# Optimization experiments

Hardware: AMD Instinct MI355X
Metric: run time of the kernel (lower is better)

The kernel has to match this reference:

```python
import jax, jax.numpy as jnp
import numpy as np

B, T, HID = 4, 2048, 2048
H, DK, DV = 16, 128, 128
EPS = 1e-5


def setup_inputs() -> dict:
    key = jax.random.key(0)
    ks = jax.random.split(key, 14)
    w = lambda k, shape, s=0.02: jax.random.normal(k, shape, jnp.float32) * s
    return dict(
        hidden_states=jax.random.normal(ks[0], (B, T, HID), jnp.float32),
        recurrent_state=jnp.zeros((B, H, DK, DV), jnp.float32),
        q_w=w(ks[1], (H * DK, HID)),
        k_w=w(ks[2], (H * DK, HID)),
        v_w=w(ks[3], (H * DV, HID)),
        f_w0=w(ks[4], (DV, HID)),
        f_w1=w(ks[5], (H * DK, DV)),
        b_w=w(ks[6], (H, HID)),
        A_log=jnp.log(jax.random.uniform(ks[7], (H,), jnp.float32, 1.0, 16.0)),
        dt_bias=w(ks[8], (H * DK,), 0.1),
        g_w0=w(ks[9], (DV, HID)),
        g_w1=w(ks[10], (H * DV, DV)),
        g_b1=w(ks[11], (H * DV,), 0.1),
        o_norm_weight=jnp.ones((DV,), jnp.float32),
        o_w=w(ks[12], (HID, H * DV)),
    )


def _l2norm(x):
    return x * jax.lax.rsqrt(jnp.sum(x * x, -1, keepdims=True) + 1e-6)


def _kda_scan(q, k, v, g, beta, S0):
    # time-major inputs: q,k,g [T,B,H,DK]; v [T,B,H,DV]; beta [T,B,H]; S0 [B,H,DK,DV]
    scale = DK ** -0.5

    def step(S, inp):
        qt, kt, vt, gt, bt = inp
        S = S * jnp.exp(gt)[..., None]                      # per-key-dim decay
        kv = jnp.einsum('bhk,bhkv->bhv', kt, S)             # current readout for k
        delta = (vt - kv) * bt[..., None]                   # beta-weighted correction
        S = S + kt[..., :, None] * delta[..., None, :]      # rank-1 delta update
        ot = jnp.einsum('bhk,bhkv->bhv', qt * scale, S)
        return S, ot

    S, o = jax.lax.scan(step, S0, (q, k, v, g, beta))
    return o, S


def reference(hidden_states, recurrent_state, q_w, k_w, v_w, f_w0, f_w1, b_w,
              A_log, dt_bias, g_w0, g_w1, g_b1, o_norm_weight, o_w):
    h = hidden_states
    q = jax.nn.silu(h @ q_w.T).reshape(B, T, H, DK)
    k = jax.nn.silu(h @ k_w.T).reshape(B, T, H, DK)
    v = jax.nn.silu(h @ v_w.T).reshape(B, T, H, DV)
    # fused_kda_gate: g = -exp(A_log) * softplus(g + dt_bias), per key channel
    g = ((h @ f_w0.T) @ f_w1.T).reshape(B, T, H, DK)
    g = -jnp.exp(A_log)[None, None, :, None] * jax.nn.softplus(g + dt_bias.reshape(H, DK))
    beta = jax.nn.sigmoid(h @ b_w.T)  # [B,T,H]
    q = _l2norm(q)
    k = _l2norm(k)
    tm = lambda x: jnp.swapaxes(x, 0, 1)  # -> time-major
    o, S = _kda_scan(tm(q), tm(k), tm(v), tm(g), tm(beta), recurrent_state)
    o = jnp.swapaxes(o, 0, 1)  # [B,T,H,DV]
    factor = ((h @ g_w0.T) @ g_w1.T + g_b1).reshape(B, T, H, DV)
    # FusedRMSNormGated(activation='sigmoid'): rmsnorm then sigmoid gate
    o = o * jax.lax.rsqrt(jnp.mean(o * o, -1, keepdims=True) + EPS)
    o = o * o_norm_weight * jax.nn.sigmoid(factor)
    out = o.reshape(B, T, H * DV) @ o_w.T
    return out, S
```

## Files before the change

kernel.cpp:

```cpp
#include <hip/hip_runtime.h>
#include <math.h>


typedef short short8 __attribute__((ext_vector_type(8)));
typedef float f32x4 __attribute__((ext_vector_type(4)));
typedef unsigned short ushort_t;

enum { ACT_NONE = 0, ACT_SILU = 1, ACT_SIGMOID = 2, ACT_KDAGATE_EXP = 3 };

__device__ __forceinline__ unsigned short f32_to_bf16(float f) {
  unsigned int u = __float_as_uint(f);
  u += 0x7FFFu + ((u >> 16) & 1u);
  return (unsigned short)(u >> 16);
}

__device__ __forceinline__ float epi_act(float x, int act, int n,
                                         const float* bias, const float* A_log,
                                         const float* dt_bias) {
  if (bias) x += bias[n];
  if (act == ACT_SILU) {
    x = x / (1.f + __expf(-x));
  } else if (act == ACT_SIGMOID) {
    x = 1.f / (1.f + __expf(-x));
  } else if (act == ACT_KDAGATE_EXP) {
    float y = x + dt_bias[n];
    float sp = fmaxf(y, 0.f) + log1pf(__expf(-fabsf(y)));
    x = __expf(-__expf(A_log[n >> 7]) * sp);
  }
  return x;
}

__device__ __forceinline__ void gld_lds16(const void* g, void* l) {
  __builtin_amdgcn_global_load_lds(
      (const __attribute__((address_space(1))) unsigned int*)g,
      (__attribute__((address_space(3))) unsigned int*)l, 16, 0, 0);
}

__device__ __forceinline__ float row16_sum(float x) {
  x += __int_as_float(__builtin_amdgcn_update_dpp(0, __float_as_int(x), 0xB1, 0xF, 0xF, true));
  x += __int_as_float(__builtin_amdgcn_update_dpp(0, __float_as_int(x), 0x4E, 0xF, 0xF, true));
  x += __int_as_float(__builtin_amdgcn_update_dpp(0, __float_as_int(x), 0x141, 0xF, 0xF, true));
  x += __int_as_float(__builtin_amdgcn_update_dpp(0, __float_as_int(x), 0x140, 0xF, 0xF, true));
  return x;
}

__device__ __forceinline__ void unpk8(const uint4 p, float* f) {
  f[0] = __uint_as_float(p.x << 16); f[1] = __uint_as_float(p.x & 0xFFFF0000u);
  f[2] = __uint_as_float(p.y << 16); f[3] = __uint_as_float(p.y & 0xFFFF0000u);
  f[4] = __uint_as_float(p.z << 16); f[5] = __uint_as_float(p.z & 0xFFFF0000u);
  f[6] = __uint_as_float(p.w << 16); f[7] = __uint_as_float(p.w & 0xFFFF0000u);
}

__global__ __launch_bounds__(256) void gemm_bf16_nt(
    const ushort_t* __restrict__ A, const ushort_t* __restrict__ W,
    float* __restrict__ Cf, ushort_t* __restrict__ Cb,
    int M, int N, int K, int act, const float* __restrict__ bias,
    const float* __restrict__ A_log, const float* __restrict__ dt_bias) {
  __shared__ alignas(16) ushort_t As[4096];
  __shared__ alignas(16) ushort_t Bs[4096];
  const int tid = threadIdx.x;
  const int wv = tid >> 6, ln = tid & 63;
  const int bm = blockIdx.y * 128, bn = blockIdx.x * 128;
  const int wm = wv >> 1, wn = wv & 1;

  const int srow = tid >> 2;
  const int skg = (tid & 3) ^ ((srow >> 1) & 3);
  const size_t ag0 = (size_t)(bm + srow) * K + skg * 8;
  const size_t ag1 = ag0 + (size_t)64 * K;
  const size_t bg0 = (size_t)(bn + srow) * K + skg * 8;
  const size_t bg1 = bg0 + (size_t)64 * K;
  char* const lA = (char*)As;
  char* const lB = (char*)Bs;
  const int wbase = wv * 1024;

  const int fr = ln & 15, fq = ln >> 4;
  const int pg = fq ^ ((fr >> 1) & 3);
  int aoff[4], boff[4];
#pragma unroll
  for (int i = 0; i < 4; i++) {
    aoff[i] = (wm * 64 + i * 16 + fr) * 64 + pg * 16;
    boff[i] = (wn * 64 + i * 16 + fr) * 64 + pg * 16;
  }

  f32x4 acc[4][4];
#pragma unroll
  for (int i = 0; i < 4; i++)
#pragma unroll
    for (int j = 0; j < 4; j++) {
      acc[i][j][0] = 0.f; acc[i][j][1] = 0.f; acc[i][j][2] = 0.f; acc[i][j][3] = 0.f;
    }

  for (int k0 = 0; k0 < K; k0 += 32) {
    gld_lds16(A + ag0 + k0, lA + wbase);
    gld_lds16(A + ag1 + k0, lA + 4096 + wbase);
    gld_lds16(W + bg0 + k0, lB + wbase);
    gld_lds16(W + bg1 + k0, lB + 4096 + wbase);
    __syncthreads();
    short8 af[4], bf[4];
#pragma unroll
    for (int i = 0; i < 4; i++) af[i] = *(const short8*)(lA + aoff[i]);
#pragma unroll
    for (int i = 0; i < 4; i++) bf[i] = *(const short8*)(lB + boff[i]);
#pragma unroll
    for (int i = 0; i < 4; i++)
#pragma unroll
      for (int j = 0; j < 4; j++)
        acc[i][j] = __builtin_amdgcn_mfma_f32_16x16x32_bf16(af[i], bf[j], acc[i][j], 0, 0, 0);
    __syncthreads();
  }

  const int cc = ln & 15, cq = ln >> 4;
#pragma unroll
  for (int i = 0; i < 4; i++) {
#pragma unroll
    for (int r = 0; r < 4; r++) {
      const int gm = bm + wm * 64 + i * 16 + cq * 4 + r;
#pragma unroll
      for (int j = 0; j < 4; j++) {
        const int gn = bn + wn * 64 + j * 16 + cc;
        float x = epi_act(acc[i][j][r], act, gn, bias, A_log, dt_bias);
        if (Cb) Cb[(size_t)gm * N + gn] = f32_to_bf16(x);
        else    Cf[(size_t)gm * N + gn] = x;
      }
    }
  }
}

#define BM 128
#define BN 128
#define BKK 8
__global__ __launch_bounds__(256) void gemm_nt(
    const float* __restrict__ A, const float* __restrict__ W,
    float* __restrict__ C, int M, int N, int K, int act) {
  __shared__ alignas(16) float Asf[BKK][BM + 4];
  __shared__ alignas(16) float Wsf[BKK][BN + 4];
  const int tid = threadIdx.x;
  const int bm = blockIdx.y * BM;
  const int bn = blockIdx.x * BN;
  const int tn = tid & 15, tm = tid >> 4;
  const int lrow = tid >> 1;
  const int lk = (tid & 1) * 4;

  float acc[8][8];
#pragma unroll
  for (int i = 0; i < 8; i++)
#pragma unroll
    for (int j = 0; j < 8; j++) acc[i][j] = 0.f;

  for (int k0 = 0; k0 < K; k0 += BKK) {
    const float4 a4 = *(const float4*)&A[(size_t)(bm + lrow) * K + k0 + lk];
    float4 w4 = make_float4(0.f, 0.f, 0.f, 0.f);
    if (bn + lrow < N) w4 = *(const float4*)&W[(size_t)(bn + lrow) * K + k0 + lk];
    __syncthreads();
    Asf[lk + 0][lrow] = a4.x; Asf[lk + 1][lrow] = a4.y;
    Asf[lk + 2][lrow] = a4.z; Asf[lk + 3][lrow] = a4.w;
    Wsf[lk + 0][lrow] = w4.x; Wsf[lk + 1][lrow] = w4.y;
    Wsf[lk + 2][lrow] = w4.z; Wsf[lk + 3][lrow] = w4.w;
    __syncthreads();
#pragma unroll
    for (int kk = 0; kk < BKK; kk++) {
      const float4 a0 = *(const float4*)&Asf[kk][tm * 8];
      const float4 a1 = *(const float4*)&Asf[kk][tm * 8 + 4];
      const float4 b0 = *(const float4*)&Wsf[kk][tn * 8];
      const float4 b1 = *(const float4*)&Wsf[kk][tn * 8 + 4];
      const float av[8] = {a0.x, a0.y, a0.z, a0.w, a1.x, a1.y, a1.z, a1.w};
      const float bv[8] = {b0.x, b0.y, b0.z, b0.w, b1.x, b1.y, b1.z, b1.w};
#pragma unroll
      for (int i = 0; i < 8; i++)
#pragma unroll
        for (int j = 0; j < 8; j++) acc[i][j] = fmaf(av[i], bv[j], acc[i][j]);
    }
  }
#pragma unroll
  for (int i = 0; i < 8; i++) {
    const int m = bm + tm * 8 + i;
#pragma unroll
    for (int j = 0; j < 8; j++) {
      const int n = bn + tn * 8 + j;
      if (n < N) {
        float x = acc[i][j];
        if (act == ACT_SIGMOID) x = 1.f / (1.f + __expf(-x));
        C[(size_t)m * N + n] = x;
      }
    }
  }
}

__global__ __launch_bounds__(256) void cast_bf16(const float* __restrict__ x,
                                                 ushort_t* __restrict__ y, int n) {
  const int i = (blockIdx.x * 256 + threadIdx.x) * 4;
  if (i >= n) return;
  const float4 v = *(const float4*)&x[i];
  union { ushort_t u[4]; uint2 v2; } o;
  o.u[0] = f32_to_bf16(v.x); o.u[1] = f32_to_bf16(v.y);
  o.u[2] = f32_to_bf16(v.z); o.u[3] = f32_to_bf16(v.w);
  *(uint2*)&y[i] = o.v2;
}

__global__ __launch_bounds__(64) void l2norm_bf16(const float* __restrict__ x,
                                                  ushort_t* __restrict__ y, float scale) {
  const size_t base = (size_t)blockIdx.x * 128;
  const int lane = threadIdx.x;
  const float a = x[base + lane];
  const float b = x[base + lane + 64];
  float ss = fmaf(a, a, b * b);
#pragma unroll
  for (int m = 1; m < 64; m <<= 1) ss += __shfl_xor(ss, m);
  const float r = rsqrtf(ss + 1e-6f) * scale;
  y[base + lane] = f32_to_bf16(a * r);
  y[base + lane + 64] = f32_to_bf16(b * r);
}

struct StepRegs { uint4 kp, qp; float4 g0, g1; float vv, bb; };

__global__ __launch_bounds__(64) void kda_scan(
    const ushort_t* __restrict__ q, const ushort_t* __restrict__ k,
    const float* __restrict__ v, const float* __restrict__ ge,
    const float* __restrict__ beta, const float* __restrict__ S0,
    float* __restrict__ o, float* __restrict__ S_out) {
  const int bid = blockIdx.x;
  const int bh = (((bid >> 3) & 7) << 3) | (bid & 7);
  const int cg = bid >> 6;
  const int h = bh & 15, b = bh >> 4;
  const int ln = threadIdx.x;
  const int cl = ln >> 4, kg = ln & 15;
  const int col = cg * 4 + cl;
  const int kof = kg * 8;

  const size_t s_base = (size_t)bh * (128 * 128);
  float S[8];
#pragma unroll
  for (int j = 0; j < 8; j++) S[j] = S0[s_base + (size_t)(kof + j) * 128 + col];

  const size_t rb = (size_t)b * (2048 * 2048) + (size_t)h * 128;
  const size_t bbase = (size_t)(b * 2048) * 16 + h;

  StepRegs sr[4];
#pragma unroll
  for (int s = 0; s < 4; s++) {
    const size_t a = rb + (size_t)s * 2048;
    sr[s].kp = *(const uint4*)&k[a + kof];
    sr[s].qp = *(const uint4*)&q[a + kof];
    sr[s].g0 = *(const float4*)&ge[a + kof];
    sr[s].g1 = *(const float4*)&ge[a + kof + 4];
    sr[s].vv = v[a + col];
    sr[s].bb = beta[bbase + (size_t)s * 16];
  }

  for (int t = 0; t < 2048; t += 4) {
#pragma unroll
    for (int s = 0; s < 4; s++) {
      const int tt = t + s;
      float kf[8], qf[8];
      unpk8(sr[s].kp, kf);
      unpk8(sr[s].qp, qf);
      const float4 g0 = sr[s].g0, g1 = sr[s].g1;
      float p0 = 0.f, p1 = 0.f;
      S[0] *= g0.x; p0 = fmaf(kf[0], S[0], p0);
      S[1] *= g0.y; p1 = fmaf(kf[1], S[1], p1);
      S[2] *= g0.z; p0 = fmaf(kf[2], S[2], p0);
      S[3] *= g0.w; p1 = fmaf(kf[3], S[3], p1);
      S[4] *= g1.x; p0 = fmaf(kf[4], S[4], p0);
      S[5] *= g1.y; p1 = fmaf(kf[5], S[5], p1);
      S[6] *= g1.z; p0 = fmaf(kf[6], S[6], p0);
      S[7] *= g1.w; p1 = fmaf(kf[7], S[7], p1);
      const float p = row16_sum(p0 + p1);
      const float delta = (sr[s].vv - p) * sr[s].bb;
      float o0 = 0.f, o1 = 0.f;
      S[0] = fmaf(kf[0], delta, S[0]); o0 = fmaf(qf[0], S[0], o0);
      S[1] = fmaf(kf[1], delta, S[1]); o1 = fmaf(qf[1], S[1], o1);
      S[2] = fmaf(kf[2], delta, S[2]); o0 = fmaf(qf[2], S[2], o0);
      S[3] = fmaf(kf[3], delta, S[3]); o1 = fmaf(qf[3], S[3], o1);
      S[4] = fmaf(kf[4], delta, S[4]); o0 = fmaf(qf[4], S[4], o0);
      S[5] = fmaf(kf[5], delta, S[5]); o1 = fmaf(qf[5], S[5], o1);
      S[6] = fmaf(kf[6], delta, S[6]); o0 = fmaf(qf[6], S[6], o0);
      S[7] = fmaf(kf[7], delta, S[7]); o1 = fmaf(qf[7], S[7], o1);
      const float op = row16_sum(o0 + o1);
      if (kg == 0) o[rb + (size_t)tt * 2048 + col] = op;
      const int tn = (tt + 4 < 2048) ? tt + 4 : 2047;
      const size_t a = rb + (size_t)tn * 2048;
      sr[s].kp = *(const uint4*)&k[a + kof];
      sr[s].qp = *(const uint4*)&q[a + kof];
      sr[s].g0 = *(const float4*)&ge[a + kof];
      sr[s].g1 = *(const float4*)&ge[a + kof + 4];
      sr[s].vv = v[a + col];
      sr[s].bb = beta[bbase + (size_t)tn * 16];
    }
  }
#pragma unroll
  for (int j = 0; j < 8; j++)
    S_out[s_base + (size_t)(kof + j) * 128 + col] = S[j];
}

__global__ __launch_bounds__(128) void gate_rmsnorm(
    const float* __restrict__ o, const float* __restrict__ factor,
    const float* __restrict__ w, ushort_t* __restrict__ out) {
  const size_t base = (size_t)blockIdx.x * 128;
  const int vi = threadIdx.x;
  const float x = o[base + vi];
  float ss = x * x;
#pragma unroll
  for (int m = 1; m < 64; m <<= 1) ss += __shfl_xor(ss, m);
  __shared__ float red[2];
  if ((vi & 63) == 0) red[vi >> 6] = ss;
  __syncthreads();
  const float tot = red[0] + red[1];
  const float r = rsqrtf(tot * (1.f / 128.f) + 1e-5f);
  const float f = factor[base + vi];
  const float sig = 1.f / (1.f + __expf(-f));
  out[base + vi] = f32_to_bf16(x * r * w[vi] * sig);
}

extern "C" void kernel_launch(void* const* d_in, const int* in_sizes, int n_in,
                              void* d_out, int out_size, void* d_ws, size_t ws_size,
                              hipStream_t stream) {
  const float* h    = (const float*)d_in[0];
  const float* S0   = (const float*)d_in[1];
  const float* q_w  = (const float*)d_in[2];
  const float* k_w  = (const float*)d_in[3];
  const float* v_w  = (const float*)d_in[4];
  const float* f_w0 = (const float*)d_in[5];
  const float* f_w1 = (const float*)d_in[6];
  const float* b_w  = (const float*)d_in[7];
  const float* A_log  = (const float*)d_in[8];
  const float* dt_b   = (const float*)d_in[9];
  const float* g_w0 = (const float*)d_in[10];
  const float* g_w1 = (const float*)d_in[11];
  const float* g_b1 = (const float*)d_in[12];
  const float* o_nw = (const float*)d_in[13];
  const float* o_w  = (const float*)d_in[14];

  float* outp = (float*)d_out;
  float* Sout = outp + (size_t)8192 * 2048;

  const size_t BIG = (size_t)8192 * 2048;
  float* ws = (float*)d_ws;
  float* vbuf = ws;
  float* obuf = vbuf + BIG;
  float* betab = obuf + BIG;
  ushort_t* qb16 = (ushort_t*)(betab + (size_t)8192 * 16);
  ushort_t* kb16 = qb16 + BIG;
  ushort_t* hb   = kb16 + BIG;
  ushort_t* wq   = hb + BIG;
  ushort_t* wk   = wq + (size_t)2048 * 2048;
  ushort_t* wv   = wk + (size_t)2048 * 2048;
  ushort_t* wo   = wv + (size_t)2048 * 2048;
  ushort_t* wf0  = wo + (size_t)2048 * 2048;
  ushort_t* wg0  = wf0 + (size_t)128 * 2048;
  ushort_t* wf1  = wg0 + (size_t)128 * 2048;
  ushort_t* wg1  = wf1 + (size_t)2048 * 128;
  ushort_t* fpreb = wg1 + (size_t)2048 * 128;
  ushort_t* gpreb = fpreb + (size_t)8192 * 128;

  const dim3 blk(256);
  const dim3 gbig(16, 64);
  const dim3 gnarrow(1, 64);

  cast_bf16<<<16384, blk, 0, stream>>>(h, hb, 8192 * 2048);
  cast_bf16<<<4096, blk, 0, stream>>>(q_w, wq, 2048 * 2048);
  cast_bf16<<<4096, blk, 0, stream>>>(k_w, wk, 2048 * 2048);
  cast_bf16<<<4096, blk, 0, stream>>>(v_w, wv, 2048 * 2048);
  cast_bf16<<<4096, blk, 0, stream>>>(o_w, wo, 2048 * 2048);
  cast_bf16<<<256, blk, 0, stream>>>(f_w0, wf0, 128 * 2048);
  cast_bf16<<<256, blk, 0, stream>>>(g_w0, wg0, 128 * 2048);
  cast_bf16<<<256, blk, 0, stream>>>(f_w1, wf1, 2048 * 128);
  cast_bf16<<<256, blk, 0, stream>>>(g_w1, wg1, 2048 * 128);

  gemm_bf16_nt<<<gbig, blk, 0, stream>>>(hb, wq, obuf, nullptr, 8192, 2048, 2048, ACT_SILU, nullptr, nullptr, nullptr);
  l2norm_bf16<<<131072, 64, 0, stream>>>(obuf, qb16, 0.08838834764831845f);
  gemm_bf16_nt<<<gbig, blk, 0, stream>>>(hb, wk, obuf, nullptr, 8192, 2048, 2048, ACT_SILU, nullptr, nullptr, nullptr);
  l2norm_bf16<<<131072, 64, 0, stream>>>(obuf, kb16, 1.0f);
  gemm_bf16_nt<<<gbig, blk, 0, stream>>>(hb, wv, vbuf, nullptr, 8192, 2048, 2048, ACT_SILU, nullptr, nullptr, nullptr);
  gemm_bf16_nt<<<gnarrow, blk, 0, stream>>>(hb, wf0, nullptr, fpreb, 8192, 128, 2048, ACT_NONE, nullptr, nullptr, nullptr);
  gemm_bf16_nt<<<gnarrow, blk, 0, stream>>>(hb, wg0, nullptr, gpreb, 8192, 128, 2048, ACT_NONE, nullptr, nullptr, nullptr);
  gemm_nt<<<gnarrow, blk, 0, stream>>>(h, b_w, betab, 8192, 16, 2048, ACT_SIGMOID);
  gemm_bf16_nt<<<gbig, blk, 0, stream>>>(fpreb, wf1, outp, nullptr, 8192, 2048, 128, ACT_KDAGATE_EXP, nullptr, A_log, dt_b);
  kda_scan<<<2048, 64, 0, stream>>>(qb16, kb16, vbuf, outp, betab, S0, obuf, Sout);
  gemm_bf16_nt<<<gbig, blk, 0, stream>>>(gpreb, wg1, outp, nullptr, 8192, 2048, 128, ACT_NONE, g_b1, nullptr, nullptr);
  gate_rmsnorm<<<131072, 128, 0, stream>>>(obuf, outp, o_nw, qb16);
  gemm_bf16_nt<<<gbig, blk, 0, stream>>>(qb16, wo, outp, nullptr, 8192, 2048, 2048, ACT_NONE, nullptr, nullptr, nullptr);
}
```

Measured before the change: 2.130 ms.

## Fuse QKV projections with L2 norm epilogue, merge low-rank GEMMs, restructure scan

Merges the three Q/K/V projection GEMMs into one launch over concatenated weights. The SiLU and per-row L2 normalization are now done in the GEMM epilogue through an LDS cross-wave reduction, which removes the separate l2norm kernels. The f/g low-rank down-projections and the beta projection are combined into one bf16 GEMM, replacing the fp32 SIMT GEMM for beta. The scan now reads q and k as fp32 and computes the output as q·S_decayed + (q·k)·delta, so the three reductions can proceed together. The gated RMSNorm is rewritten to process several rows per block with vectorized accesses. In exchange, q and k buffers move from bf16 to fp32, which doubles their traffic in the scan.

```diff
diff --git a/kernel.cpp b/kernel.cpp
--- a/kernel.cpp
+++ b/kernel.cpp
@@ -6,7 +6,7 @@
 typedef float f32x4 __attribute__((ext_vector_type(4)));
 typedef unsigned short ushort_t;
 
-enum { ACT_NONE = 0, ACT_SILU = 1, ACT_SIGMOID = 2, ACT_KDAGATE_EXP = 3 };
+enum { M_PLAIN = 0, M_QKV = 1, M_LOWRANK = 2, M_GATE = 3, M_FACTOR = 4 };
 
 __device__ __forceinline__ unsigned short f32_to_bf16(float f) {
   unsigned int u = __float_as_uint(f);
@@ -14,21 +14,7 @@
   return (unsigned short)(u >> 16);
 }
 
-__device__ __forceinline__ float epi_act(float x, int act, int n,
-                                         const float* bias, const float* A_log,
-                                         const float* dt_bias) {
-  if (bias) x += bias[n];
-  if (act == ACT_SILU) {
-    x = x / (1.f + __expf(-x));
-  } else if (act == ACT_SIGMOID) {
-    x = 1.f / (1.f + __expf(-x));
-  } else if (act == ACT_KDAGATE_EXP) {
-    float y = x + dt_bias[n];
-    float sp = fmaxf(y, 0.f) + log1pf(__expf(-fabsf(y)));
-    x = __expf(-__expf(A_log[n >> 7]) * sp);
-  }
-  return x;
-}
+__device__ __forceinline__ float silu(float x) { return x / (1.f + __expf(-x)); }
 
 __device__ __forceinline__ void gld_lds16(const void* g, void* l) {
   __builtin_amdgcn_global_load_lds(
@@ -44,20 +30,16 @@
   return x;
 }
 
-__device__ __forceinline__ void unpk8(const uint4 p, float* f) {
-  f[0] = __uint_as_float(p.x << 16); f[1] = __uint_as_float(p.x & 0xFFFF0000u);
-  f[2] = __uint_as_float(p.y << 16); f[3] = __uint_as_float(p.y & 0xFFFF0000u);
-  f[4] = __uint_as_float(p.z << 16); f[5] = __uint_as_float(p.z & 0xFFFF0000u);
-  f[6] = __uint_as_float(p.w << 16); f[7] = __uint_as_float(p.w & 0xFFFF0000u);
-}
-
-__global__ __launch_bounds__(256) void gemm_bf16_nt(
+__global__ __launch_bounds__(256) void gemm_bf16(
     const ushort_t* __restrict__ A, const ushort_t* __restrict__ W,
-    float* __restrict__ Cf, ushort_t* __restrict__ Cb,
-    int M, int N, int K, int act, const float* __restrict__ bias,
-    const float* __restrict__ A_log, const float* __restrict__ dt_bias) {
+    int M, int N, int K, int mode,
+    float* __restrict__ f0, float* __restrict__ f1, float* __restrict__ f2,
+    ushort_t* __restrict__ b0, ushort_t* __restrict__ b1,
+    const float* __restrict__ bias, const float* __restrict__ A_log,
+    const float* __restrict__ dt_bias) {
   __shared__ alignas(16) ushort_t As[4096];
   __shared__ alignas(16) ushort_t Bs[4096];
+  __shared__ float l2s[2][128];
   const int tid = threadIdx.x;
   const int wv = tid >> 6, ln = tid & 63;
   const int bm = blockIdx.y * 128, bn = blockIdx.x * 128;
@@ -110,80 +92,94 @@
   }
 
   const int cc = ln & 15, cq = ln >> 4;
-#pragma unroll
-  for (int i = 0; i < 4; i++) {
+
+  if (mode == M_QKV) {
+#pragma unroll
+    for (int i = 0; i < 4; i++)
+#pragma unroll
+      for (int j = 0; j < 4; j++)
+#pragma unroll
+        for (int r = 0; r < 4; r++) acc[i][j][r] = silu(acc[i][j][r]);
+    const bool isqk = (bn < 4096);
+    float invr[4][4];
+    if (isqk) {
+      const float scale = (bn < 2048) ? 0.08838834764831845f : 1.0f;
+#pragma unroll
+      for (int i = 0; i < 4; i++)
+#pragma unroll
+        for (int r = 0; r < 4; r++) {
+          float ss = 0.f;
+#pragma unroll
+          for (int j = 0; j < 4; j++) ss = fmaf(acc[i][j][r], acc[i][j][r], ss);
+          ss = row16_sum(ss);
+          if (cc == 0) l2s[wn][wm * 64 + i * 16 + cq * 4 + r] = ss;
+        }
+      __syncthreads();
+#pragma unroll
+      for (int i = 0; i < 4; i++)
+#pragma unroll
+        for (int r = 0; r < 4; r++) {
+          const int rl = wm * 64 + i * 16 + cq * 4 + r;
+          invr[i][r] = rsqrtf(l2s[0][rl] + l2s[1][rl] + 1e-6f) * scale;
+        }
+    } else {
+#pragma unroll
+      for (int i = 0; i < 4; i++)
+#pragma unroll
+        for (int r = 0; r < 4; r++) invr[i][r] = 1.f;
+    }
+    float* dst = (bn < 2048) ? f0 : ((bn < 4096) ? f1 : f2);
+    const int nb = bn & 2047;
+#pragma unroll
+    for (int i = 0; i < 4; i++)
+#pragma unroll
+      for (int r = 0; r < 4; r++) {
+        const int gm = bm + wm * 64 + i * 16 + cq * 4 + r;
+#pragma unroll
+        for (int j = 0; j < 4; j++) {
+          const int gn = nb + wn * 64 + j * 16 + cc;
+          dst[(size_t)gm * 2048 + gn] = acc[i][j][r] * invr[i][r];
+        }
+      }
+    return;
+  }
+
+  if (mode == M_LOWRANK) {
+#pragma unroll
+    for (int i = 0; i < 4; i++)
+#pragma unroll
+      for (int r = 0; r < 4; r++) {
+        const int gm = bm + wm * 64 + i * 16 + cq * 4 + r;
+#pragma unroll
+        for (int j = 0; j < 4; j++) {
+          const int gn = bn + wn * 64 + j * 16 + cc;
+          const float x = acc[i][j][r];
+          if (gn < 128) b0[(size_t)gm * 128 + gn] = f32_to_bf16(x);
+          else if (gn < 256) b1[(size_t)gm * 128 + (gn - 128)] = f32_to_bf16(x);
+          else if (gn < 272) f0[(size_t)gm * 16 + (gn - 256)] = 1.f / (1.f + __expf(-x));
+        }
+      }
+    return;
+  }
+
+#pragma unroll
+  for (int i = 0; i < 4; i++)
 #pragma unroll
     for (int r = 0; r < 4; r++) {
       const int gm = bm + wm * 64 + i * 16 + cq * 4 + r;
 #pragma unroll
       for (int j = 0; j < 4; j++) {
         const int gn = bn + wn * 64 + j * 16 + cc;
-        float x = epi_act(acc[i][j][r], act, gn, bias, A_log, dt_bias);
-        if (Cb) Cb[(size_t)gm * N + gn] = f32_to_bf16(x);
-        else    Cf[(size_t)gm * N + gn] = x;
+        float x = acc[i][j][r];
+        if (mode == M_FACTOR) x += bias[gn];
+        else if (mode == M_GATE) {
+          const float y = x + dt_bias[gn];
+          const float sp = fmaxf(y, 0.f) + log1pf(__expf(-fabsf(y)));
+          x = __expf(-__expf(A_log[gn >> 7]) * sp);
+        }
+        f0[(size_t)gm * N + gn] = x;
       }
     }
-  }
-}
-
-#define BM 128
-#define BN 128
-#define BKK 8
-__global__ __launch_bounds__(256) void gemm_nt(
-    const float* __restrict__ A, const float* __restrict__ W,
-    float* __restrict__ C, int M, int N, int K, int act) {
-  __shared__ alignas(16) float Asf[BKK][BM + 4];
-  __shared__ alignas(16) float Wsf[BKK][BN + 4];
-  const int tid = threadIdx.x;
-  const int bm = blockIdx.y * BM;
-  const int bn = blockIdx.x * BN;
-  const int tn = tid & 15, tm = tid >> 4;
-  const int lrow = tid >> 1;
-  const int lk = (tid & 1) * 4;
-
-  float acc[8][8];
-#pragma unroll
-  for (int i = 0; i < 8; i++)
-#pragma unroll
-    for (int j = 0; j < 8; j++) acc[i][j] = 0.f;
-
-  for (int k0 = 0; k0 < K; k0 += BKK) {
-    const float4 a4 = *(const float4*)&A[(size_t)(bm + lrow) * K + k0 + lk];
-    float4 w4 = make_float4(0.f, 0.f, 0.f, 0.f);
-    if (bn + lrow < N) w4 = *(const float4*)&W[(size_t)(bn + lrow) * K + k0 + lk];
-    __syncthreads();
-    Asf[lk + 0][lrow] = a4.x; Asf[lk + 1][lrow] = a4.y;
-    Asf[lk + 2][lrow] = a4.z; Asf[lk + 3][lrow] = a4.w;
-    Wsf[lk + 0][lrow] = w4.x; Wsf[lk + 1][lrow] = w4.y;
-    Wsf[lk + 2][lrow] = w4.z; Wsf[lk + 3][lrow] = w4.w;
-    __syncthreads();
-#pragma unroll
-    for (int kk = 0; kk < BKK; kk++) {
-      const float4 a0 = *(const float4*)&Asf[kk][tm * 8];
-      const float4 a1 = *(const float4*)&Asf[kk][tm * 8 + 4];
-      const float4 b0 = *(const float4*)&Wsf[kk][tn * 8];
-      const float4 b1 = *(const float4*)&Wsf[kk][tn * 8 + 4];
-      const float av[8] = {a0.x, a0.y, a0.z, a0.w, a1.x, a1.y, a1.z, a1.w};
-      const float bv[8] = {b0.x, b0.y, b0.z, b0.w, b1.x, b1.y, b1.z, b1.w};
-#pragma unroll
-      for (int i = 0; i < 8; i++)
-#pragma unroll
-        for (int j = 0; j < 8; j++) acc[i][j] = fmaf(av[i], bv[j], acc[i][j]);
-    }
-  }
-#pragma unroll
-  for (int i = 0; i < 8; i++) {
-    const int m = bm + tm * 8 + i;
-#pragma unroll
-    for (int j = 0; j < 8; j++) {
-      const int n = bn + tn * 8 + j;
-      if (n < N) {
-        float x = acc[i][j];
-        if (act == ACT_SIGMOID) x = 1.f / (1.f + __expf(-x));
-        C[(size_t)m * N + n] = x;
-      }
-    }
-  }
 }
 
 __global__ __launch_bounds__(256) void cast_bf16(const float* __restrict__ x,
@@ -197,24 +193,8 @@
   *(uint2*)&y[i] = o.v2;
 }
 
-__global__ __launch_bounds__(64) void l2norm_bf16(const float* __restrict__ x,
-                                                  ushort_t* __restrict__ y, float scale) {
-  const size_t base = (size_t)blockIdx.x * 128;
-  const int lane = threadIdx.x;
-  const float a = x[base + lane];
-  const float b = x[base + lane + 64];
-  float ss = fmaf(a, a, b * b);
-#pragma unroll
-  for (int m = 1; m < 64; m <<= 1) ss += __shfl_xor(ss, m);
-  const float r = rsqrtf(ss + 1e-6f) * scale;
-  y[base + lane] = f32_to_bf16(a * r);
-  y[base + lane + 64] = f32_to_bf16(b * r);
-}
-
-struct StepRegs { uint4 kp, qp; float4 g0, g1; float vv, bb; };
-
 __global__ __launch_bounds__(64) void kda_scan(
-    const ushort_t* __restrict__ q, const ushort_t* __restrict__ k,
+    const float* __restrict__ q, const float* __restrict__ k,
     const float* __restrict__ v, const float* __restrict__ ge,
     const float* __restrict__ beta, const float* __restrict__ S0,
     float* __restrict__ o, float* __restrict__ S_out) {
@@ -235,56 +215,56 @@
   const size_t rb = (size_t)b * (2048 * 2048) + (size_t)h * 128;
   const size_t bbase = (size_t)(b * 2048) * 16 + h;
 
-  StepRegs sr[4];
+  float4 sk0[4], sk1[4], sq0[4], sq1[4], sg0[4], sg1[4];
+  float sv[4], sb[4];
 #pragma unroll
   for (int s = 0; s < 4; s++) {
     const size_t a = rb + (size_t)s * 2048;
-    sr[s].kp = *(const uint4*)&k[a + kof];
-    sr[s].qp = *(const uint4*)&q[a + kof];
-    sr[s].g0 = *(const float4*)&ge[a + kof];
-    sr[s].g1 = *(const float4*)&ge[a + kof + 4];
-    sr[s].vv = v[a + col];
-    sr[s].bb = beta[bbase + (size_t)s * 16];
+    sk0[s] = *(const float4*)&k[a + kof];  sk1[s] = *(const float4*)&k[a + kof + 4];
+    sq0[s] = *(const float4*)&q[a + kof];  sq1[s] = *(const float4*)&q[a + kof + 4];
+    sg0[s] = *(const float4*)&ge[a + kof]; sg1[s] = *(const float4*)&ge[a + kof + 4];
+    sv[s] = v[a + col];
+    sb[s] = beta[bbase + (size_t)s * 16];
   }
 
   for (int t = 0; t < 2048; t += 4) {
 #pragma unroll
     for (int s = 0; s < 4; s++) {
-      const int tt = t + s;
-      float kf[8], qf[8];
-      unpk8(sr[s].kp, kf);
-      unpk8(sr[s].qp, qf);
-      const float4 g0 = sr[s].g0, g1 = sr[s].g1;
-      float p0 = 0.f, p1 = 0.f;
-      S[0] *= g0.x; p0 = fmaf(kf[0], S[0], p0);
-      S[1] *= g0.y; p1 = fmaf(kf[1], S[1], p1);
-      S[2] *= g0.z; p0 = fmaf(kf[2], S[2], p0);
-      S[3] *= g0.w; p1 = fmaf(kf[3], S[3], p1);
-      S[4] *= g1.x; p0 = fmaf(kf[4], S[4], p0);
-      S[5] *= g1.y; p1 = fmaf(kf[5], S[5], p1);
-      S[6] *= g1.z; p0 = fmaf(kf[6], S[6], p0);
-      S[7] *= g1.w; p1 = fmaf(kf[7], S[7], p1);
-      const float p = row16_sum(p0 + p1);
-      const float delta = (sr[s].vv - p) * sr[s].bb;
-      float o0 = 0.f, o1 = 0.f;
-      S[0] = fmaf(kf[0], delta, S[0]); o0 = fmaf(qf[0], S[0], o0);
-      S[1] = fmaf(kf[1], delta, S[1]); o1 = fmaf(qf[1], S[1], o1);
-      S[2] = fmaf(kf[2], delta, S[2]); o0 = fmaf(qf[2], S[2], o0);
-      S[3] = fmaf(kf[3], delta, S[3]); o1 = fmaf(qf[3], S[3], o1);
-      S[4] = fmaf(kf[4], delta, S[4]); o0 = fmaf(qf[4], S[4], o0);
-      S[5] = fmaf(kf[5], delta, S[5]); o1 = fmaf(qf[5], S[5], o1);
-      S[6] = fmaf(kf[6], delta, S[6]); o0 = fmaf(qf[6], S[6], o0);
-      S[7] = fmaf(kf[7], delta, S[7]); o1 = fmaf(qf[7], S[7], o1);
-      const float op = row16_sum(o0 + o1);
-      if (kg == 0) o[rb + (size_t)tt * 2048 + col] = op;
-      const int tn = (tt + 4 < 2048) ? tt + 4 : 2047;
-      const size_t a = rb + (size_t)tn * 2048;
-      sr[s].kp = *(const uint4*)&k[a + kof];
-      sr[s].qp = *(const uint4*)&q[a + kof];
-      sr[s].g0 = *(const float4*)&ge[a + kof];
-      sr[s].g1 = *(const float4*)&ge[a + kof + 4];
-      sr[s].vv = v[a + col];
-      sr[s].bb = beta[bbase + (size_t)tn * 16];
+      const float4 K0 = sk0[s], K1 = sk1[s], Q0 = sq0[s], Q1 = sq1[s];
+      const float4 G0 = sg0[s], G1 = sg1[s];
+      const float VV = sv[s], BB = sb[s];
+      {
+        int tn = t + s + 4; if (tn > 2047) tn = 2047;
+        const size_t a = rb + (size_t)tn * 2048;
+        sk0[s] = *(const float4*)&k[a + kof];  sk1[s] = *(const float4*)&k[a + kof + 4];
+        sq0[s] = *(const float4*)&q[a + kof];  sq1[s] = *(const float4*)&q[a + kof + 4];
+        sg0[s] = *(const float4*)&ge[a + kof]; sg1[s] = *(const float4*)&ge[a + kof + 4];
+        sv[s] = v[a + col];
+        sb[s] = beta[bbase + (size_t)tn * 16];
+      }
+      float p0 = 0.f, p1 = 0.f, o0 = 0.f, o1 = 0.f, d0 = 0.f, d1 = 0.f;
+      S[0] *= G0.x; p0 = fmaf(K0.x, S[0], p0); o0 = fmaf(Q0.x, S[0], o0); d0 = fmaf(Q0.x, K0.x, d0);
+      S[1] *= G0.y; p1 = fmaf(K0.y, S[1], p1); o1 = fmaf(Q0.y, S[1], o1); d1 = fmaf(Q0.y, K0.y, d1);
+      S[2] *= G0.z; p0 = fmaf(K0.z, S[2], p0); o0 = fmaf(Q0.z, S[2], o0); d0 = fmaf(Q0.z, K0.z, d0);
+      S[3] *= G0.w; p1 = fmaf(K0.w, S[3], p1); o1 = fmaf(Q0.w, S[3], o1); d1 = fmaf(Q0.w, K0.w, d1);
+      S[4] *= G1.x; p0 = fmaf(K1.x, S[4], p0); o0 = fmaf(Q1.x, S[4], o0); d0 = fmaf(Q1.x, K1.x, d0);
+      S[5] *= G1.y; p1 = fmaf(K1.y, S[5], p1); o1 = fmaf(Q1.y, S[5], o1); d1 = fmaf(Q1.y, K1.y, d1);
+      S[6] *= G1.z; p0 = fmaf(K1.z, S[6], p0); o0 = fmaf(Q1.z, S[6], o0); d0 = fmaf(Q1.z, K1.z, d0);
+      S[7] *= G1.w; p1 = fmaf(K1.w, S[7], p1); o1 = fmaf(Q1.w, S[7], o1); d1 = fmaf(Q1.w, K1.w, d1);
+      const float p  = row16_sum(p0 + p1);
+      const float oq = row16_sum(o0 + o1);
+      const float qk = row16_sum(d0 + d1);
+      const float delta = (VV - p) * BB;
+      const float op = fmaf(qk, delta, oq);
+      if (kg == 0) o[rb + (size_t)(t + s) * 2048 + col] = op;
+      S[0] = fmaf(K0.x, delta, S[0]);
+      S[1] = fmaf(K0.y, delta, S[1]);
+      S[2] = fmaf(K0.z, delta, S[2]);
+      S[3] = fmaf(K0.w, delta, S[3]);
+      S[4] = fmaf(K1.x, delta, S[4]);
+      S[5] = fmaf(K1.y, delta, S[5]);
+      S[6] = fmaf(K1.z, delta, S[6]);
+      S[7] = fmaf(K1.w, delta, S[7]);
     }
   }
 #pragma unroll
@@ -292,23 +272,26 @@
     S_out[s_base + (size_t)(kof + j) * 128 + col] = S[j];
 }
 
-__global__ __launch_bounds__(128) void gate_rmsnorm(
+__global__ __launch_bounds__(256) void gate_rmsnorm(
     const float* __restrict__ o, const float* __restrict__ factor,
     const float* __restrict__ w, ushort_t* __restrict__ out) {
-  const size_t base = (size_t)blockIdx.x * 128;
-  const int vi = threadIdx.x;
-  const float x = o[base + vi];
-  float ss = x * x;
-#pragma unroll
-  for (int m = 1; m < 64; m <<= 1) ss += __shfl_xor(ss, m);
-  __shared__ float red[2];
-  if ((vi & 63) == 0) red[vi >> 6] = ss;
-  __syncthreads();
-  const float tot = red[0] + red[1];
-  const float r = rsqrtf(tot * (1.f / 128.f) + 1e-5f);
-  const float f = factor[base + vi];
-  const float sig = 1.f / (1.f + __expf(-f));
-  out[base + vi] = f32_to_bf16(x * r * w[vi] * sig);
+  const int ln = threadIdx.x & 63, wv = threadIdx.x >> 6;
+  const float w0 = w[ln * 2], w1 = w[ln * 2 + 1];
+  const size_t row0 = (size_t)blockIdx.x * 64 + wv * 16;
+  for (int it = 0; it < 16; it++) {
+    const size_t base = (row0 + it) * 128 + ln * 2;
+    const float2 x = *(const float2*)&o[base];
+    const float2 f = *(const float2*)&factor[base];
+    float ss = fmaf(x.x, x.x, x.y * x.y);
+    ss = row16_sum(ss);
+    ss += __shfl_xor(ss, 16);
+    ss += __shfl_xor(ss, 32);
+    const float r = rsqrtf(ss * (1.f / 128.f) + 1e-5f);
+    const float y0 = x.x * r * w0 / (1.f + __expf(-f.x));
+    const float y1 = x.y * r * w1 / (1.f + __expf(-f.y));
+    *(unsigned int*)&out[base] =
+        (unsigned int)f32_to_bf16(y0) | ((unsigned int)f32_to_bf16(y1) << 16);
+  }
 }
 
 extern "C" void kernel_launch(void* const* d_in, const int* in_sizes, int n_in,
@@ -335,48 +318,44 @@
 
   const size_t BIG = (size_t)8192 * 2048;
   float* ws = (float*)d_ws;
-  float* vbuf = ws;
-  float* obuf = vbuf + BIG;
-  float* betab = obuf + BIG;
-  ushort_t* qb16 = (ushort_t*)(betab + (size_t)8192 * 16);
-  ushort_t* kb16 = qb16 + BIG;
-  ushort_t* hb   = kb16 + BIG;
-  ushort_t* wq   = hb + BIG;
-  ushort_t* wk   = wq + (size_t)2048 * 2048;
-  ushort_t* wv   = wk + (size_t)2048 * 2048;
-  ushort_t* wo   = wv + (size_t)2048 * 2048;
-  ushort_t* wf0  = wo + (size_t)2048 * 2048;
-  ushort_t* wg0  = wf0 + (size_t)128 * 2048;
-  ushort_t* wf1  = wg0 + (size_t)128 * 2048;
-  ushort_t* wg1  = wf1 + (size_t)2048 * 128;
-  ushort_t* fpreb = wg1 + (size_t)2048 * 128;
+  float* vbuf  = ws;
+  float* qbuf  = vbuf + BIG;
+  float* kbuf  = qbuf + BIG;
+  float* betab = kbuf + BIG;
+  ushort_t* fpreb = (ushort_t*)(betab + (size_t)8192 * 16);
   ushort_t* gpreb = fpreb + (size_t)8192 * 128;
+  ushort_t* wf1   = gpreb + (size_t)8192 * 128;
+  ushort_t* wg1   = wf1 + (size_t)2048 * 128;
+  ushort_t* wo    = wg1 + (size_t)2048 * 128;
+  ushort_t* wlow  = wo + (size_t)2048 * 2048;
+  ushort_t* hb    = wlow + (size_t)384 * 2048;
+  ushort_t* wqkv  = hb + BIG;
+  float* obuf = (float*)hb;
+  ushort_t* gatedb = (ushort_t*)qbuf;
 
   const dim3 blk(256);
-  const dim3 gbig(16, 64);
-  const dim3 gnarrow(1, 64);
 
   cast_bf16<<<16384, blk, 0, stream>>>(h, hb, 8192 * 2048);
-  cast_bf16<<<4096, blk, 0, stream>>>(q_w, wq, 2048 * 2048);
-  cast_bf16<<<4096, blk, 0, stream>>>(k_w, wk, 2048 * 2048);
-  cast_bf16<<<4096, blk, 0, stream>>>(v_w, wv, 2048 * 2048);
+  cast_bf16<<<4096, blk, 0, stream>>>(q_w, wqkv, 2048 * 2048);
+  cast_bf16<<<4096, blk, 0, stream>>>(k_w, wqkv + (size_t)2048 * 2048, 2048 * 2048);
+  cast_bf16<<<4096, blk, 0, stream>>>(v_w, wqkv + (size_t)4096 * 2048, 2048 * 2048);
   cast_bf16<<<4096, blk, 0, stream>>>(o_w, wo, 2048 * 2048);
-  cast_bf16<<<256, blk, 0, stream>>>(f_w0, wf0, 128 * 2048);
-  cast_bf16<<<256, blk, 0, stream>>>(g_w0, wg0, 128 * 2048);
+  cast_bf16<<<256, blk, 0, stream>>>(f_w0, wlow, 128 * 2048);
+  cast_bf16<<<256, blk, 0, stream>>>(g_w0, wlow + (size_t)128 * 2048, 128 * 2048);
+  cast_bf16<<<32, blk, 0, stream>>>(b_w, wlow + (size_t)256 * 2048, 16 * 2048);
   cast_bf16<<<256, blk, 0, stream>>>(f_w1, wf1, 2048 * 128);
   cast_bf16<<<256, blk, 0, stream>>>(g_w1, wg1, 2048 * 128);
 
-  gemm_bf16_nt<<<gbig, blk, 0, stream>>>(hb, wq, obuf, nullptr, 8192, 2048, 2048, ACT_SILU, nullptr, nullptr, nullptr);
-  l2norm_bf16<<<131072, 64, 0, stream>>>(obuf, qb16, 0.08838834764831845f);
-  gemm_bf16_nt<<<gbig, blk, 0, stream>>>(hb, wk, obuf, nullptr, 8192, 2048, 2048, ACT_SILU, nullptr, nullptr, nullptr);
-  l2norm_bf16<<<131072, 64, 0, stream>>>(obuf, kb16, 1.0f);
-  gemm_bf16_nt<<<gbig, blk, 0, stream>>>(hb, wv, vbuf, nullptr, 8192, 2048, 2048, ACT_SILU, nullptr, nullptr, nullptr);
-  gemm_bf16_nt<<<gnarrow, blk, 0, stream>>>(hb, wf0, nullptr, fpreb, 8192, 128, 2048, ACT_NONE, nullptr, nullptr, nullptr);
-  gemm_bf16_nt<<<gnarrow, blk, 0, stream>>>(hb, wg0, nullptr, gpreb, 8192, 128, 2048, ACT_NONE, nullptr, nullptr, nullptr);
-  gemm_nt<<<gnarrow, blk, 0, stream>>>(h, b_w, betab, 8192, 16, 2048, ACT_SIGMOID);
-  gemm_bf16_nt<<<gbig, blk, 0, stream>>>(fpreb, wf1, outp, nullptr, 8192, 2048, 128, ACT_KDAGATE_EXP, nullptr, A_log, dt_b);
-  kda_scan<<<2048, 64, 0, stream>>>(qb16, kb16, vbuf, outp, betab, S0, obuf, Sout);
-  gemm_bf16_nt<<<gbig, blk, 0, stream>>>(gpreb, wg1, outp, nullptr, 8192, 2048, 128, ACT_NONE, g_b1, nullptr, nullptr);
-  gate_rmsnorm<<<131072, 128, 0, stream>>>(obuf, outp, o_nw, qb16);
-  gemm_bf16_nt<<<gbig, blk, 0, stream>>>(qb16, wo, outp, nullptr, 8192, 2048, 2048, ACT_NONE, nullptr, nullptr, nullptr);
-}
+  gemm_bf16<<<dim3(48, 64), blk, 0, stream>>>(hb, wqkv, 8192, 6144, 2048, M_QKV,
+      qbuf, kbuf, vbuf, nullptr, nullptr, nullptr, nullptr, nullptr);
+  gemm_bf16<<<dim3(3, 64), blk, 0, stream>>>(hb, wlow, 8192, 384, 2048, M_LOWRANK,
+      betab, nullptr, nullptr, fpreb, gpreb, nullptr, nullptr, nullptr);
+  gemm_bf16<<<dim3(16, 64), blk, 0, stream>>>(fpreb, wf1, 8192, 2048, 128, M_GATE,
+      outp, nullptr, nullptr, nullptr, nullptr, nullptr, A_log, dt_b);
+  kda_scan<<<2048, 64, 0, stream>>>(qbuf, kbuf, vbuf, outp, betab, S0, obuf, Sout);
+  gemm_bf16<<<dim3(16, 64), blk, 0, stream>>>(gpreb, wg1, 8192, 2048, 128, M_FACTOR,
+      outp, nullptr, nullptr, nullptr, nullptr, g_b1, nullptr, nullptr);
+  gate_rmsnorm<<<2048, blk, 0, stream>>>(obuf, outp, o_nw, gatedb);
+  gemm_bf16<<<dim3(16, 64), blk, 0, stream>>>(gatedb, wo, 8192, 2048, 2048, M_PLAIN,
+      outp, nullptr, nullptr, nullptr, nullptr, nullptr, nullptr, nullptr);
+}
```

Result: no change. 2.093 ms (-1.8%).
